# Kernel optimization log

Measured on AMD Instinct MI355X. Metric: run time of the kernel, lower is better.

The kernel has to match this reference:

```python
import jax, jax.numpy as jnp
import numpy as np

N, K = 16384, 16
SIZE, DIST = 256, 64
HEADS, ATTN = 8, 32
HIDDEN = 512
HA = HEADS * ATTN  # 256
EDGE = SIZE + DIST  # key/value input size per edge


def setup_inputs() -> dict:
    key = jax.random.key(0)
    ks = jax.random.split(key, 16)
    s = lambda k, fi, fo: jax.random.normal(k, (fi, fo), jnp.float32) / np.sqrt(fi)
    return {
        "features": jax.random.normal(ks[0], (N, SIZE), jnp.float32),
        "distances": jax.random.normal(ks[1], (N, K, DIST), jnp.float32),
        "structure": jax.random.randint(ks[2], (N, K), 0, N, jnp.int32),
        # local MLP: size -> hidden -> hidden -> size (depth=3 linears)
        "W0": s(ks[3], SIZE, HIDDEN), "b0": jnp.zeros((HIDDEN,), jnp.float32),
        "W1": s(ks[4], HIDDEN, HIDDEN), "b1": jnp.zeros((HIDDEN,), jnp.float32),
        "W2": s(ks[5], HIDDEN, SIZE), "b2": jnp.zeros((SIZE,), jnp.float32),
        # neighbour dot multi-head attention
        "Wq": s(ks[6], SIZE, HA), "bq": jnp.zeros((HA,), jnp.float32),
        "Wk": s(ks[7], EDGE, HA), "bk": jnp.zeros((HA,), jnp.float32),
        "Wv": s(ks[8], EDGE, HA), "bv": jnp.zeros((HA,), jnp.float32),
        "Wo": s(ks[9], HA, SIZE), "bo": jnp.zeros((SIZE,), jnp.float32),
    }


def reference(features, distances, structure,
              W0, b0, W1, b1, W2, b2,
              Wq, bq, Wk, bk, Wv, bv, Wo, bo):
    # batch_norm=False -> bn layers are identity; activation = relu
    inputs = jax.nn.relu(features)                      # [N, size]
    # local MLP (ReLU between layers), then outer activation
    h = jax.nn.relu(inputs @ W0 + b0)
    h = jax.nn.relu(h @ W1 + b1)
    local = jax.nn.relu(h @ W2 + b2)                    # [N, size]
    # edge structure: gather neighbour features, concat distance features
    neigh = local[structure]                            # [N, K, size]
    edge = jnp.concatenate([neigh, distances], axis=-1) # [N, K, size+dist]
    # neighbour-restricted multi-head dot attention
    q = (features @ Wq + bq).reshape(N, HEADS, ATTN)    # [N, H, A]
    k = (edge @ Wk + bk).reshape(N, K, HEADS, ATTN)     # [N, K, H, A]
    v = (edge @ Wv + bv).reshape(N, K, HEADS, ATTN)
    scale = jnp.float32(1.0 / np.sqrt(ATTN))
    scores = jnp.einsum('nha,nkha->nhk', q, k) * scale  # [N, H, K]
    attn = jax.nn.softmax(scores, axis=-1)
    o = jnp.einsum('nhk,nkha->nha', attn, v).reshape(N, HA)
    out = o @ Wo + bo                                   # [N, size]
    return features + out
```

## Files before the change

kernel.cpp:

```cpp
#include <hip/hip_runtime.h>
#include <hip/hip_bf16.h>

#define NN 16384
#define SIZE 256
#define DISTD 64
#define KNBR 16
#define HEADS 8
#define HIDDEN 512
#define HA 256
#define SCALE 0.17677669529663687f

typedef __bf16 bf16;
typedef bf16 bf16x2 __attribute__((ext_vector_type(2)));
typedef bf16 bf16x4 __attribute__((ext_vector_type(4)));
typedef bf16 bf16x8 __attribute__((ext_vector_type(8)));
typedef float f32x4 __attribute__((ext_vector_type(4)));

__device__ __forceinline__ void gload16(const void* g, void* l) {
    __builtin_amdgcn_global_load_lds(
        (const __attribute__((address_space(1))) unsigned int*)g,
        (__attribute__((address_space(3))) unsigned int*)l, 16, 0, 0);
}

template<bool BIAS, bool RELU_OUT, bool RESID, typename OutT>
__global__ __launch_bounds__(256) void gemm128(
    const bf16* __restrict__ A, const bf16* __restrict__ BT,
    const float* __restrict__ bias, const float* __restrict__ resid,
    OutT* __restrict__ C, int M, int N, int K)
{
    __shared__ alignas(16) bf16 As[2][128][32];
    __shared__ alignas(16) bf16 Bs[2][128][32];

    const int t = threadIdx.x;
    const int w = t >> 6, l = t & 63;
    const int bm = blockIdx.y * 128, bn = blockIdx.x * 128;
    const int wr = (w >> 1) * 64, wc = (w & 1) * 64;

    f32x4 acc[4][4] = {};

    const bf16* ag = A  + (size_t)(bm + (t >> 2)) * K + (t & 3) * 8;
    const bf16* bg = BT + (size_t)(bn + (t >> 2)) * K + (t & 3) * 8;

    const int nt = K >> 5;
    {
        bf16* asl = &As[0][w << 4][0];
        bf16* bsl = &Bs[0][w << 4][0];
        gload16(ag, asl);
        gload16(ag + (size_t)64 * K, (char*)asl + 4096);
        gload16(bg, bsl);
        gload16(bg + (size_t)64 * K, (char*)bsl + 4096);
    }
    __syncthreads();

    for (int tt = 0; tt < nt; ++tt) {
        const int cur = tt & 1;
        if (tt + 1 < nt) {
            const int k0 = (tt + 1) << 5;
            bf16* asl = &As[cur ^ 1][w << 4][0];
            bf16* bsl = &Bs[cur ^ 1][w << 4][0];
            gload16(ag + k0, asl);
            gload16(ag + k0 + (size_t)64 * K, (char*)asl + 4096);
            gload16(bg + k0, bsl);
            gload16(bg + k0 + (size_t)64 * K, (char*)bsl + 4096);
        }
        bf16x8 af[4], bfr[4];
        #pragma unroll
        for (int m = 0; m < 4; ++m)
            af[m] = *(const bf16x8*)&As[cur][wr + m * 16 + (l & 15)][(l >> 4) * 8];
        #pragma unroll
        for (int n2 = 0; n2 < 4; ++n2)
            bfr[n2] = *(const bf16x8*)&Bs[cur][wc + n2 * 16 + (l & 15)][(l >> 4) * 8];
        #pragma unroll
        for (int m = 0; m < 4; ++m)
            #pragma unroll
            for (int n2 = 0; n2 < 4; ++n2)
                acc[m][n2] = __builtin_amdgcn_mfma_f32_16x16x32_bf16(
                    af[m], bfr[n2], acc[m][n2], 0, 0, 0);
        __syncthreads();
    }

    #pragma unroll
    for (int m = 0; m < 4; ++m) {
        const int row = bm + wr + m * 16 + ((l >> 4) << 2);
        #pragma unroll
        for (int n2 = 0; n2 < 4; ++n2) {
            const int col = bn + wc + n2 * 16 + (l & 15);
            #pragma unroll
            for (int i = 0; i < 4; ++i) {
                float v = acc[m][n2][i];
                if (BIAS) v += bias[col];
                if (RESID) v += resid[(size_t)(row + i) * N + col];
                if (RELU_OUT) v = fmaxf(v, 0.f);
                C[(size_t)(row + i) * N + col] = (OutT)v;
            }
        }
    }
}

__global__ __launch_bounds__(256) void g1qcat_kernel(
    const bf16* __restrict__ fbf, const bf16* __restrict__ frbf,
    const bf16* __restrict__ W0T, const float* __restrict__ b0,
    const bf16* __restrict__ WqcatT, const float* __restrict__ bqcat,
    bf16* __restrict__ H0, bf16* __restrict__ qbf, float* __restrict__ qprojF)
{
    __shared__ alignas(16) bf16 As[2][128][32];
    __shared__ alignas(16) bf16 Bs[2][128][32];

    const int bx = blockIdx.x, by = blockIdx.y;
    const bool isG1 = bx < 4;
    const int cx = bx - 4;
    const bf16* A  = isG1 ? frbf : fbf;
    const bf16* BT = isG1 ? (W0T + (size_t)bx * 128 * 256)
                          : (WqcatT + (size_t)cx * 128 * 256);
    const float* bias = isG1 ? (b0 + bx * 128) : (bqcat + cx * 128);
    const int K = 256;

    const int t = threadIdx.x;
    const int w = t >> 6, l = t & 63;
    const int bm = by * 128;
    const int wr = (w >> 1) * 64, wc = (w & 1) * 64;

    f32x4 acc[4][4] = {};

    const bf16* ag = A  + (size_t)(bm + (t >> 2)) * K + (t & 3) * 8;
    const bf16* bg = BT + (size_t)(t >> 2) * K + (t & 3) * 8;

    {
        bf16* asl = &As[0][w << 4][0];
        bf16* bsl = &Bs[0][w << 4][0];
        gload16(ag, asl);
        gload16(ag + (size_t)64 * K, (char*)asl + 4096);
        gload16(bg, bsl);
        gload16(bg + (size_t)64 * K, (char*)bsl + 4096);
    }
    __syncthreads();

    for (int tt = 0; tt < 8; ++tt) {
        const int cur = tt & 1;
        if (tt + 1 < 8) {
            const int k0 = (tt + 1) << 5;
            bf16* asl = &As[cur ^ 1][w << 4][0];
            bf16* bsl = &Bs[cur ^ 1][w << 4][0];
            gload16(ag + k0, asl);
            gload16(ag + k0 + (size_t)64 * K, (char*)asl + 4096);
            gload16(bg + k0, bsl);
            gload16(bg + k0 + (size_t)64 * K, (char*)bsl + 4096);
        }
        bf16x8 af[4], bfr[4];
        #pragma unroll
        for (int m = 0; m < 4; ++m)
            af[m] = *(const bf16x8*)&As[cur][wr + m * 16 + (l & 15)][(l >> 4) * 8];
        #pragma unroll
        for (int n2 = 0; n2 < 4; ++n2)
            bfr[n2] = *(const bf16x8*)&Bs[cur][wc + n2 * 16 + (l & 15)][(l >> 4) * 8];
        #pragma unroll
        for (int m = 0; m < 4; ++m)
            #pragma unroll
            for (int n2 = 0; n2 < 4; ++n2)
                acc[m][n2] = __builtin_amdgcn_mfma_f32_16x16x32_bf16(
                    af[m], bfr[n2], acc[m][n2], 0, 0, 0);
        __syncthreads();
    }

    #pragma unroll
    for (int m = 0; m < 4; ++m) {
        const int lrow = wr + m * 16 + ((l >> 4) << 2);
        #pragma unroll
        for (int n2 = 0; n2 < 4; ++n2) {
            const int lcol = wc + n2 * 16 + (l & 15);
            #pragma unroll
            for (int i = 0; i < 4; ++i) {
                float v = acc[m][n2][i] + bias[lcol];
                const size_t row = bm + lrow + i;
                if (isG1) {
                    H0[row * 512 + bx * 128 + lcol] = (bf16)fmaxf(v, 0.f);
                } else if (cx < 2) {
                    qbf[row * 256 + cx * 128 + lcol] = (bf16)v;
                } else {
                    qprojF[row * 512 + (cx - 2) * 128 + lcol] = v;
                }
            }
        }
    }
}

__global__ __launch_bounds__(256) void prep_all(
    const float* __restrict__ features,
    const float* __restrict__ W0, const float* __restrict__ W1,
    const float* __restrict__ W2, const float* __restrict__ Wq,
    const float* __restrict__ bq, const float* __restrict__ Wk,
    const float* __restrict__ Wv, const float* __restrict__ Wo,
    const float* __restrict__ bo, const float* __restrict__ bv,
    bf16* __restrict__ fbf, bf16* __restrict__ frbf,
    bf16* __restrict__ W0T, bf16* __restrict__ W1T, bf16* __restrict__ W2T,
    bf16* __restrict__ WkvT, bf16* __restrict__ WqcatT, bf16* __restrict__ WstackT,
    float* __restrict__ bqcat, float* __restrict__ biaso)
{
    if (blockIdx.x < 4096) {
        int id = blockIdx.x * 256 + threadIdx.x;
        float4 v = ((const float4*)features)[id];
        bf16x4 a, r;
        a[0] = (bf16)v.x; a[1] = (bf16)v.y; a[2] = (bf16)v.z; a[3] = (bf16)v.w;
        r[0] = (bf16)fmaxf(v.x, 0.f); r[1] = (bf16)fmaxf(v.y, 0.f);
        r[2] = (bf16)fmaxf(v.z, 0.f); r[3] = (bf16)fmaxf(v.w, 0.f);
        ((bf16x4*)fbf)[id] = a; ((bf16x4*)frbf)[id] = r;
        return;
    }
    long id = (blockIdx.x - 4096) * 256L + threadIdx.x;
    if (id < 131072) {
        int n = id >> 8, k = id & 255;
        W0T[id] = (bf16)W0[(long)k * 512 + n]; return;
    }
    id -= 131072;
    if (id < 262144) {
        int n = id >> 9, k = id & 511;
        W1T[id] = (bf16)W1[(long)k * 512 + n]; return;
    }
    id -= 262144;
    if (id < 131072) {
        int n = id >> 9, k = id & 511;
        W2T[id] = (bf16)W2[(long)k * 256 + n]; return;
    }
    id -= 131072;
    if (id < 131072) {
        int n = id >> 8, k = id & 255;
        WkvT[id] = (bf16)(n < 256 ? Wk[(long)k * 256 + n] : Wv[(long)k * 256 + (n - 256)]);
        return;
    }
    id -= 131072;
    if (id < 196608) {
        int col = id >> 8, c = id & 255;
        float s;
        if (col < 256) s = Wq[(long)c * 256 + col];
        else {
            int hd = col - 256, h = hd >> 6, d = hd & 63;
            s = 0.f;
            #pragma unroll
            for (int a = 0; a < 32; ++a)
                s += Wq[(long)c * 256 + h * 32 + a] * Wk[(long)(256 + d) * 256 + h * 32 + a];
        }
        WqcatT[id] = (bf16)(s * SCALE); return;
    }
    id -= 196608;
    if (id < 196608) {
        int col = (int)(id / 768), r = (int)(id % 768);
        float s;
        if (r < 256) s = Wo[(long)r * 256 + col];
        else {
            int hd = r - 256, h = hd >> 6, d = hd & 63;
            s = 0.f;
            #pragma unroll
            for (int a = 0; a < 32; ++a)
                s += Wv[(long)(256 + d) * 256 + h * 32 + a] * Wo[(long)(h * 32 + a) * 256 + col];
        }
        WstackT[id] = (bf16)s; return;
    }
    id -= 196608;
    if (id < 768) {
        float s;
        if (id < 256) s = bq[id];
        else {
            int hd = (int)id - 256, h = hd >> 6, d = hd & 63;
            s = 0.f;
            #pragma unroll
            for (int a = 0; a < 32; ++a)
                s += bq[h * 32 + a] * Wk[(long)(256 + d) * 256 + h * 32 + a];
        }
        bqcat[id] = s * SCALE; return;
    }
    id -= 768;
    if (id < 256) {
        float s = bo[id];
        for (int u = 0; u < 256; ++u) s += bv[u] * Wo[(long)u * 256 + id];
        biaso[id] = s;
    }
}

__global__ __launch_bounds__(256) void attn_kernel(
    const bf16*  __restrict__ qbf,
    const float* __restrict__ qprojF,
    const bf16*  __restrict__ localKV,
    const float* __restrict__ dist,
    const int*   __restrict__ structure,
    bf16* __restrict__ concat)
{
    const int n = blockIdx.x;
    const int t = threadIdx.x;
    const int h = t >> 5, j = (t >> 1) & 15, part = t & 1;

    __shared__ float dist_s[16][68];
    __shared__ bf16  V_s[16][264];
    __shared__ float attn_s[8][16];
    __shared__ int   s_s[16];

    {
        const float* dp = dist + (long)n * (KNBR * DISTD);
        #pragma unroll
        for (int i = 0; i < 4; ++i) {
            int e = i * 256 + t;
            dist_s[e >> 6][e & 63] = dp[e];
        }
    }
    if (t < 16) s_s[t] = structure[(long)n * KNBR + t];
    __syncthreads();

    #pragma unroll
    for (int pass = 0; pass < 2; ++pass) {
        int idx = pass * 256 + t;
        int row = idx >> 5, chunk = idx & 31;
        bf16x8 v = *(const bf16x8*)(localKV + (long)s_s[row] * 512 + 256 + chunk * 8);
        *(bf16x8*)&V_s[row][chunk * 8] = v;
    }

    const bf16* qq = qbf + (long)n * 256 + h * 32 + part * 16;
    bf16x8 qa = *(const bf16x8*)qq;
    bf16x8 qb = *(const bf16x8*)(qq + 8);
    const float* qpp = qprojF + (long)n * 512 + h * 64 + part * 32;
    float4 qp4[8];
    #pragma unroll
    for (int i = 0; i < 8; ++i) qp4[i] = ((const float4*)qpp)[i];

    const bf16* kp = localKV + (long)s_s[j] * 512 + h * 32 + part * 16;
    bf16x8 ka = *(const bf16x8*)kp;
    bf16x8 kb = *(const bf16x8*)(kp + 8);

    float sc = 0.f;
    #pragma unroll
    for (int i = 0; i < 8; ++i)
        sc += (float)qa[i] * (float)ka[i] + (float)qb[i] * (float)kb[i];

    const int dbase = part * 32;
    #pragma unroll
    for (int i = 0; i < 8; ++i) {
        sc += dist_s[j][dbase + 4 * i + 0] * qp4[i].x;
        sc += dist_s[j][dbase + 4 * i + 1] * qp4[i].y;
        sc += dist_s[j][dbase + 4 * i + 2] * qp4[i].z;
        sc += dist_s[j][dbase + 4 * i + 3] * qp4[i].w;
    }

    sc += __shfl_xor(sc, 1);
    float m = sc;
    m = fmaxf(m, __shfl_xor(m, 2));
    m = fmaxf(m, __shfl_xor(m, 4));
    m = fmaxf(m, __shfl_xor(m, 8));
    m = fmaxf(m, __shfl_xor(m, 16));
    float e = __expf(sc - m);
    float sum = e;
    sum += __shfl_xor(sum, 2);
    sum += __shfl_xor(sum, 4);
    sum += __shfl_xor(sum, 8);
    sum += __shfl_xor(sum, 16);
    float attn = e / sum;
    if (!part) attn_s[h][j] = attn;
    __syncthreads();

    if (t < 128) {
        const int c0 = t * 2;
        const int hh = t >> 4;
        float a0 = 0.f, a1 = 0.f;
        #pragma unroll
        for (int j2 = 0; j2 < 16; ++j2) {
            float wgt = attn_s[hh][j2];
            bf16x2 pv = *(const bf16x2*)&V_s[j2][c0];
            a0 += wgt * (float)pv[0];
            a1 += wgt * (float)pv[1];
        }
        bf16x2 o2; o2[0] = (bf16)a0; o2[1] = (bf16)a1;
        *(bf16x2*)&concat[(long)n * 768 + c0] = o2;
    } else {
        const int u = t - 128;
        const int base = u * 4;
        const int h3 = u >> 4, d3 = (u & 15) * 4;
        f32x4 acc4 = {};
        #pragma unroll
        for (int j2 = 0; j2 < 16; ++j2) {
            float wgt = attn_s[h3][j2];
            const f32x4 dv = *(const f32x4*)&dist_s[j2][d3];
            acc4 += wgt * dv;
        }
        bf16x4 o4;
        #pragma unroll
        for (int i = 0; i < 4; ++i) o4[i] = (bf16)acc4[i];
        *(bf16x4*)&concat[(long)n * 768 + 256 + base] = o4;
    }
}

extern "C" void kernel_launch(void* const* d_in, const int* in_sizes, int n_in,
                              void* d_out, int out_size, void* d_ws, size_t ws_size,
                              hipStream_t stream)
{
    const float* features = (const float*)d_in[0];
    const float* dist     = (const float*)d_in[1];
    const int*   structure= (const int*)d_in[2];
    const float* W0 = (const float*)d_in[3];
    const float* b0 = (const float*)d_in[4];
    const float* W1 = (const float*)d_in[5];
    const float* b1 = (const float*)d_in[6];
    const float* W2 = (const float*)d_in[7];
    const float* b2 = (const float*)d_in[8];
    const float* Wq = (const float*)d_in[9];
    const float* bq = (const float*)d_in[10];
    const float* Wk = (const float*)d_in[11];
    const float* Wv = (const float*)d_in[13];
    const float* bv = (const float*)d_in[14];
    const float* Wo = (const float*)d_in[15];
    const float* bo = (const float*)d_in[16];
    float* out = (float*)d_out;

    const size_t MB = 1u << 20;
    char* w = (char*)d_ws;
    float* qprojF  = (float*)(w + 0 * MB);
    bf16*  qbf     = (bf16*)(w + 32 * MB);
    bf16*  H0      = (bf16*)(w + 40 * MB);
    bf16*  local_b = (bf16*)(w + 40 * MB);
    bf16*  concat  = (bf16*)(w + 48 * MB);
    bf16*  fbf     = (bf16*)(w + 56 * MB);
    bf16*  frbf    = (bf16*)(w + 64 * MB);
    bf16*  H1      = (bf16*)(w + 56 * MB);
    bf16*  localKV = (bf16*)(w + 72 * MB);
    char*  wb      = w + 88 * MB;
    bf16*  W0T     = (bf16*)(wb + 0);
    bf16*  W1T     = (bf16*)(wb + 262144);
    bf16*  W2T     = (bf16*)(wb + 786432);
    bf16*  WkvT    = (bf16*)(wb + 1048576);
    bf16*  WqcatT  = (bf16*)(wb + 1310720);
    bf16*  WstackT = (bf16*)(wb + 1703936);
    float* bqcat   = (float*)(wb + 2097152);
    float* biaso   = (float*)(wb + 2100224);

    dim3 blk(256);

    prep_all<<<dim3(8196), blk, 0, stream>>>(
        features, W0, W1, W2, Wq, bq, Wk, Wv, Wo, bo, bv,
        fbf, frbf, W0T, W1T, W2T, WkvT, WqcatT, WstackT, bqcat, biaso);

    g1qcat_kernel<<<dim3(10, 128), blk, 0, stream>>>(
        fbf, frbf, W0T, b0, WqcatT, bqcat, H0, qbf, qprojF);

    gemm128<true,  true,  false, bf16><<<dim3(4, 128), blk, 0, stream>>>(
        H0, W1T, b1, nullptr, H1, NN, 512, 512);
    gemm128<true,  true,  false, bf16><<<dim3(2, 128), blk, 0, stream>>>(
        H1, W2T, b2, nullptr, local_b, NN, 256, 512);

    gemm128<false, false, false, bf16><<<dim3(4, 128), blk, 0, stream>>>(
        local_b, WkvT, nullptr, nullptr, localKV, NN, 512, 256);

    attn_kernel<<<dim3(NN), blk, 0, stream>>>(
        qbf, qprojF, localKV, dist, structure, concat);

    gemm128<true,  false, true,  float><<<dim3(2, 128), blk, 0, stream>>>(
        concat, WstackT, biaso, features, out, NN, 256, 768);
}
```

Baseline: 180.0 us.

## Use 128x64 GEMM tiles, store q projection in bf16, and simplify attention output

The GEMMs gain a TN template parameter and are launched with 128x64 tiles, which doubles the number of blocks so more CUs are kept busy at N=16384. The q projection for the distance term is now stored as bf16 inside one combined qcat buffer instead of fp32, cutting the bytes the attention kernel reads. The attention output phase now has every thread compute one V column plus two distance columns, and the workspace layout is compacted. Trade-offs are lower precision in the distance-score term and less data reuse per GEMM tile.

```diff
diff --git a/kernel.cpp b/kernel.cpp
--- a/kernel.cpp
+++ b/kernel.cpp
@@ -22,21 +22,22 @@
         (__attribute__((address_space(3))) unsigned int*)l, 16, 0, 0);
 }
 
-template<bool BIAS, bool RELU_OUT, bool RESID, typename OutT>
+template<bool BIAS, bool RELU_OUT, bool RESID, typename OutT, int TN>
 __global__ __launch_bounds__(256) void gemm128(
     const bf16* __restrict__ A, const bf16* __restrict__ BT,
     const float* __restrict__ bias, const float* __restrict__ resid,
     OutT* __restrict__ C, int M, int N, int K)
 {
+    constexpr int NF = TN / 32;
     __shared__ alignas(16) bf16 As[2][128][32];
-    __shared__ alignas(16) bf16 Bs[2][128][32];
+    __shared__ alignas(16) bf16 Bs[2][TN][32];
 
     const int t = threadIdx.x;
     const int w = t >> 6, l = t & 63;
-    const int bm = blockIdx.y * 128, bn = blockIdx.x * 128;
-    const int wr = (w >> 1) * 64, wc = (w & 1) * 64;
-
-    f32x4 acc[4][4] = {};
+    const int bm = blockIdx.y * 128, bn = blockIdx.x * TN;
+    const int wr = (w >> 1) * 64, wc = (w & 1) * (TN / 2);
+
+    f32x4 acc[4][NF] = {};
 
     const bf16* ag = A  + (size_t)(bm + (t >> 2)) * K + (t & 3) * 8;
     const bf16* bg = BT + (size_t)(bn + (t >> 2)) * K + (t & 3) * 8;
@@ -48,7 +49,8 @@
         gload16(ag, asl);
         gload16(ag + (size_t)64 * K, (char*)asl + 4096);
         gload16(bg, bsl);
-        gload16(bg + (size_t)64 * K, (char*)bsl + 4096);
+        if constexpr (TN == 128)
+            gload16(bg + (size_t)64 * K, (char*)bsl + 4096);
     }
     __syncthreads();
 
@@ -61,19 +63,20 @@
             gload16(ag + k0, asl);
             gload16(ag + k0 + (size_t)64 * K, (char*)asl + 4096);
             gload16(bg + k0, bsl);
-            gload16(bg + k0 + (size_t)64 * K, (char*)bsl + 4096);
-        }
-        bf16x8 af[4], bfr[4];
+            if constexpr (TN == 128)
+                gload16(bg + k0 + (size_t)64 * K, (char*)bsl + 4096);
+        }
+        bf16x8 af[4], bfr[NF];
         #pragma unroll
         for (int m = 0; m < 4; ++m)
             af[m] = *(const bf16x8*)&As[cur][wr + m * 16 + (l & 15)][(l >> 4) * 8];
         #pragma unroll
-        for (int n2 = 0; n2 < 4; ++n2)
+        for (int n2 = 0; n2 < NF; ++n2)
             bfr[n2] = *(const bf16x8*)&Bs[cur][wc + n2 * 16 + (l & 15)][(l >> 4) * 8];
         #pragma unroll
         for (int m = 0; m < 4; ++m)
             #pragma unroll
-            for (int n2 = 0; n2 < 4; ++n2)
+            for (int n2 = 0; n2 < NF; ++n2)
                 acc[m][n2] = __builtin_amdgcn_mfma_f32_16x16x32_bf16(
                     af[m], bfr[n2], acc[m][n2], 0, 0, 0);
         __syncthreads();
@@ -83,7 +86,7 @@
     for (int m = 0; m < 4; ++m) {
         const int row = bm + wr + m * 16 + ((l >> 4) << 2);
         #pragma unroll
-        for (int n2 = 0; n2 < 4; ++n2) {
+        for (int n2 = 0; n2 < NF; ++n2) {
             const int col = bn + wc + n2 * 16 + (l & 15);
             #pragma unroll
             for (int i = 0; i < 4; ++i) {
@@ -101,7 +104,7 @@
     const bf16* __restrict__ fbf, const bf16* __restrict__ frbf,
     const bf16* __restrict__ W0T, const float* __restrict__ b0,
     const bf16* __restrict__ WqcatT, const float* __restrict__ bqcat,
-    bf16* __restrict__ H0, bf16* __restrict__ qbf, float* __restrict__ qprojF)
+    bf16* __restrict__ H0, bf16* __restrict__ qcat)
 {
     __shared__ alignas(16) bf16 As[2][128][32];
     __shared__ alignas(16) bf16 Bs[2][128][32];
@@ -174,10 +177,8 @@
                 const size_t row = bm + lrow + i;
                 if (isG1) {
                     H0[row * 512 + bx * 128 + lcol] = (bf16)fmaxf(v, 0.f);
-                } else if (cx < 2) {
-                    qbf[row * 256 + cx * 128 + lcol] = (bf16)v;
                 } else {
-                    qprojF[row * 512 + (cx - 2) * 128 + lcol] = v;
+                    qcat[row * 768 + cx * 128 + lcol] = (bf16)v;
                 }
             }
         }
@@ -277,18 +278,17 @@
 }
 
 __global__ __launch_bounds__(256) void attn_kernel(
-    const bf16*  __restrict__ qbf,
-    const float* __restrict__ qprojF,
-    const bf16*  __restrict__ localKV,
+    const bf16* __restrict__ qcat,
+    const bf16* __restrict__ localKV,
     const float* __restrict__ dist,
-    const int*   __restrict__ structure,
+    const int*  __restrict__ structure,
     bf16* __restrict__ concat)
 {
     const int n = blockIdx.x;
     const int t = threadIdx.x;
     const int h = t >> 5, j = (t >> 1) & 15, part = t & 1;
 
-    __shared__ float dist_s[16][68];
+    __shared__ float dist_s[16][65];
     __shared__ bf16  V_s[16][264];
     __shared__ float attn_s[8][16];
     __shared__ int   s_s[16];
@@ -312,14 +312,14 @@
         *(bf16x8*)&V_s[row][chunk * 8] = v;
     }
 
-    const bf16* qq = qbf + (long)n * 256 + h * 32 + part * 16;
-    bf16x8 qa = *(const bf16x8*)qq;
-    bf16x8 qb = *(const bf16x8*)(qq + 8);
-    const float* qpp = qprojF + (long)n * 512 + h * 64 + part * 32;
-    float4 qp4[8];
-    #pragma unroll
-    for (int i = 0; i < 8; ++i) qp4[i] = ((const float4*)qpp)[i];
-
+    const bf16* qp_q = qcat + (long)n * 768 + h * 32 + part * 16;
+    bf16x8 qa = *(const bf16x8*)qp_q;
+    bf16x8 qb = *(const bf16x8*)(qp_q + 8);
+    const bf16* qp_p = qcat + (long)n * 768 + 256 + h * 64 + part * 32;
+    bf16x8 p0 = *(const bf16x8*)qp_p;
+    bf16x8 p1 = *(const bf16x8*)(qp_p + 8);
+    bf16x8 p2 = *(const bf16x8*)(qp_p + 16);
+    bf16x8 p3 = *(const bf16x8*)(qp_p + 24);
     const bf16* kp = localKV + (long)s_s[j] * 512 + h * 32 + part * 16;
     bf16x8 ka = *(const bf16x8*)kp;
     bf16x8 kb = *(const bf16x8*)(kp + 8);
@@ -331,12 +331,13 @@
 
     const int dbase = part * 32;
     #pragma unroll
-    for (int i = 0; i < 8; ++i) {
-        sc += dist_s[j][dbase + 4 * i + 0] * qp4[i].x;
-        sc += dist_s[j][dbase + 4 * i + 1] * qp4[i].y;
-        sc += dist_s[j][dbase + 4 * i + 2] * qp4[i].z;
-        sc += dist_s[j][dbase + 4 * i + 3] * qp4[i].w;
-    }
+    for (int i = 0; i < 8; ++i) sc += dist_s[j][dbase + i]      * (float)p0[i];
+    #pragma unroll
+    for (int i = 0; i < 8; ++i) sc += dist_s[j][dbase + 8 + i]  * (float)p1[i];
+    #pragma unroll
+    for (int i = 0; i < 8; ++i) sc += dist_s[j][dbase + 16 + i] * (float)p2[i];
+    #pragma unroll
+    for (int i = 0; i < 8; ++i) sc += dist_s[j][dbase + 24 + i] * (float)p3[i];
 
     sc += __shfl_xor(sc, 1);
     float m = sc;
@@ -354,34 +355,21 @@
     if (!part) attn_s[h][j] = attn;
     __syncthreads();
 
-    if (t < 128) {
-        const int c0 = t * 2;
-        const int hh = t >> 4;
-        float a0 = 0.f, a1 = 0.f;
-        #pragma unroll
-        for (int j2 = 0; j2 < 16; ++j2) {
-            float wgt = attn_s[hh][j2];
-            bf16x2 pv = *(const bf16x2*)&V_s[j2][c0];
-            a0 += wgt * (float)pv[0];
-            a1 += wgt * (float)pv[1];
-        }
-        bf16x2 o2; o2[0] = (bf16)a0; o2[1] = (bf16)a1;
-        *(bf16x2*)&concat[(long)n * 768 + c0] = o2;
-    } else {
-        const int u = t - 128;
-        const int base = u * 4;
-        const int h3 = u >> 4, d3 = (u & 15) * 4;
-        f32x4 acc4 = {};
-        #pragma unroll
-        for (int j2 = 0; j2 < 16; ++j2) {
-            float wgt = attn_s[h3][j2];
-            const f32x4 dv = *(const f32x4*)&dist_s[j2][d3];
-            acc4 += wgt * dv;
-        }
-        bf16x4 o4;
-        #pragma unroll
-        for (int i = 0; i < 4; ++i) o4[i] = (bf16)acc4[i];
-        *(bf16x4*)&concat[(long)n * 768 + 256 + base] = o4;
+    float acc = 0.f;
+    #pragma unroll
+    for (int j2 = 0; j2 < 16; ++j2)
+        acc += attn_s[h][j2] * (float)V_s[j2][t];
+    concat[(long)n * 768 + t] = (bf16)acc;
+
+    #pragma unroll
+    for (int rep = 0; rep < 2; ++rep) {
+        int idx = rep * 256 + t;
+        int h3 = idx >> 6, d3 = idx & 63;
+        float s2 = 0.f;
+        #pragma unroll
+        for (int j2 = 0; j2 < 16; ++j2)
+            s2 += attn_s[h3][j2] * dist_s[j2][d3];
+        concat[(long)n * 768 + 256 + idx] = (bf16)s2;
     }
 }
 
@@ -409,16 +397,15 @@
 
     const size_t MB = 1u << 20;
     char* w = (char*)d_ws;
-    float* qprojF  = (float*)(w + 0 * MB);
-    bf16*  qbf     = (bf16*)(w + 32 * MB);
-    bf16*  H0      = (bf16*)(w + 40 * MB);
-    bf16*  local_b = (bf16*)(w + 40 * MB);
-    bf16*  concat  = (bf16*)(w + 48 * MB);
-    bf16*  fbf     = (bf16*)(w + 56 * MB);
-    bf16*  frbf    = (bf16*)(w + 64 * MB);
+    bf16*  fbf     = (bf16*)(w + 0 * MB);
+    bf16*  local_b = (bf16*)(w + 0 * MB);
+    bf16*  frbf    = (bf16*)(w + 8 * MB);
+    bf16*  localKV = (bf16*)(w + 8 * MB);
+    bf16*  H0      = (bf16*)(w + 16 * MB);
+    bf16*  qcat    = (bf16*)(w + 32 * MB);
     bf16*  H1      = (bf16*)(w + 56 * MB);
-    bf16*  localKV = (bf16*)(w + 72 * MB);
-    char*  wb      = w + 88 * MB;
+    bf16*  concat  = (bf16*)(w + 56 * MB);
+    char*  wb      = w + 80 * MB;
     bf16*  W0T     = (bf16*)(wb + 0);
     bf16*  W1T     = (bf16*)(wb + 262144);
     bf16*  W2T     = (bf16*)(wb + 786432);
@@ -435,19 +422,18 @@
         fbf, frbf, W0T, W1T, W2T, WkvT, WqcatT, WstackT, bqcat, biaso);
 
     g1qcat_kernel<<<dim3(10, 128), blk, 0, stream>>>(
-        fbf, frbf, W0T, b0, WqcatT, bqcat, H0, qbf, qprojF);
-
-    gemm128<true,  true,  false, bf16><<<dim3(4, 128), blk, 0, stream>>>(
+        fbf, frbf, W0T, b0, WqcatT, bqcat, H0, qcat);
+
+    gemm128<true,  true,  false, bf16, 64><<<dim3(8, 128), blk, 0, stream>>>(
         H0, W1T, b1, nullptr, H1, NN, 512, 512);
-    gemm128<true,  true,  false, bf16><<<dim3(2, 128), blk, 0, stream>>>(
+    gemm128<true,  true,  false, bf16, 64><<<dim3(4, 128), blk, 0, stream>>>(
         H1, W2T, b2, nullptr, local_b, NN, 256, 512);
-
-    gemm128<false, false, false, bf16><<<dim3(4, 128), blk, 0, stream>>>(
+    gemm128<false, false, false, bf16, 64><<<dim3(8, 128), blk, 0, stream>>>(
         local_b, WkvT, nullptr, nullptr, localKV, NN, 512, 256);
 
     attn_kernel<<<dim3(NN), blk, 0, stream>>>(
-        qbf, qprojF, localKV, dist, structure, concat);
-
-    gemm128<true,  false, true,  float><<<dim3(2, 128), blk, 0, stream>>>(
+        qcat, localKV, dist, structure, concat);
+
+    gemm128<true,  false, true,  float, 64><<<dim3(4, 128), blk, 0, stream>>>(
         concat, WstackT, biaso, features, out, NN, 256, 768);
 }
```

New measurement: 178.1 us. Within noise of the previous version (-1.1%).
